# Kernel tuning notes

Measured on AMD Instinct MI355X. Metric: run time of the kernel, lower is better.

## Reference

```python
import jax, jax.numpy as jnp
import numpy as np

B, L, DMQ, DMV = 8, 1024, 512, 512
H, DK, DV, DOUT = 8, 64, 64, 512
EPS = 1e-6


def _layer_norm(x, gamma, beta):
    # LayerNorm over last dim (size H*DK or H*DV), eps=1e-6
    mu = jnp.mean(x, axis=-1, keepdims=True)
    var = jnp.mean(jnp.square(x - mu), axis=-1, keepdims=True)
    return (x - mu) * jax.lax.rsqrt(var + EPS) * gamma + beta


def setup_inputs() -> dict:
    key = jax.random.key(0)
    ks = jax.random.split(key, 20)
    s = 0.02
    return {
        "q": jax.random.normal(ks[0], (B, L, DMQ), jnp.float32),
        "k": jax.random.normal(ks[1], (B, L, DMV), jnp.float32),
        "v": jax.random.normal(ks[2], (B, L, DMV), jnp.float32),
        "Wq": jax.random.normal(ks[3], (DMQ, H * DK), jnp.float32) * s,
        "bq": jnp.zeros((H * DK,), jnp.float32),
        "Wk": jax.random.normal(ks[4], (DMV, H * DK), jnp.float32) * s,
        "bk": jnp.zeros((H * DK,), jnp.float32),
        "Wv": jax.random.normal(ks[5], (DMV, H * DV), jnp.float32) * s,
        "bv": jnp.zeros((H * DV,), jnp.float32),
        "g_q": jnp.ones((H * DK,), jnp.float32),
        "be_q": jnp.zeros((H * DK,), jnp.float32),
        "g_k": jnp.ones((H * DK,), jnp.float32),
        "be_k": jnp.zeros((H * DK,), jnp.float32),
        "g_v": jnp.ones((H * DV,), jnp.float32),
        "be_v": jnp.zeros((H * DV,), jnp.float32),
        "W1": jax.random.normal(ks[6], (H * DV, H * DV), jnp.float32) * s,
        "b1": jnp.zeros((H * DV,), jnp.float32),
        "W2": jax.random.normal(ks[7], (H * DV, DOUT), jnp.float32) * s,
        "b2": jnp.zeros((DOUT,), jnp.float32),
    }


def reference(q, k, v, Wq, bq, Wk, bk, Wv, bv, g_q, be_q, g_k, be_k, g_v, be_v, W1, b1, W2, b2):
    b, lq = q.shape[0], q.shape[1]
    qp = q @ Wq + bq                       # [B, Lq, H*DK]
    kp = k @ Wk + bk                       # [B, Lk, H*DK]
    vp = v @ Wv + bv                       # [B, Lv, H*DV]
    residual = qp.reshape(b, lq, H, DK)
    qn = _layer_norm(qp, g_q, be_q).reshape(b, lq, H, DK)
    kn = _layer_norm(kp, g_k, be_k).reshape(b, -1, H, DK)
    vn = _layer_norm(vp, g_v, be_v).reshape(b, -1, H, DV)
    # scaled dot-product attention (mask=None path)
    scores = jnp.einsum("bqhd,bkhd->bhqk", qn, kn) / jnp.sqrt(jnp.float32(DK))
    attn = jax.nn.softmax(scores, axis=-1)
    out = jnp.einsum("bhqk,bkhd->bqhd", attn, vn).reshape(b, lq, H * DV)
    # 2-layer FFN head: fc1 (ReLU) then fc2
    h = jax.nn.relu(out @ W1 + b1)
    out = h @ W2 + b2                      # [B, Lq, DOUT]
    return (out, residual)
```

## Files before the change

### kernel.cpp

```cpp
#include <hip/hip_runtime.h>
#include <hip/hip_bf16.h>
#include <stdint.h>

typedef unsigned short u16;
typedef __attribute__((ext_vector_type(8))) short bf16x8;
typedef __attribute__((ext_vector_type(4))) float f32x4;
typedef __attribute__((ext_vector_type(16))) float f32x16;

#define NR 8192
#define DM 512
#define NH 8
#define HD 64
#define LQ 1024

#define QSCALE (0.125f * 1.4426950408889634f)
#define SOFF 16.0f

__device__ __forceinline__ u16 f2b(float f) {
    union { float f; uint32_t u; } v; v.f = f;
    uint32_t r = v.u + 0x7fffu + ((v.u >> 16) & 1u);
    return (u16)(r >> 16);
}
__device__ __forceinline__ uint32_t pk2(float lo, float hi) {
    __hip_bfloat162 h = __float22bfloat162_rn(make_float2(lo, hi));
    union { __hip_bfloat162 h; uint32_t u; } c; c.h = h;
    return c.u;
}
__device__ __forceinline__ float b2f(uint32_t lo16) {
    union { uint32_t u; float f; } c; c.u = lo16 << 16; return c.f;
}

__global__ __launch_bounds__(256)
void prep_kernel(const float* __restrict__ q, const float* __restrict__ k,
                 const float* __restrict__ v, u16* __restrict__ qo,
                 u16* __restrict__ ko, u16* __restrict__ vo,
                 const float* __restrict__ W0, const float* __restrict__ W1,
                 const float* __restrict__ W2, const float* __restrict__ W3,
                 const float* __restrict__ W4,
                 u16* __restrict__ T0, u16* __restrict__ T1, u16* __restrict__ T2,
                 u16* __restrict__ T3, u16* __restrict__ T4)
{
    __shared__ float S[64][65];
    const int bid = blockIdx.x;
    if (bid < 6144) {
        const int y = bid >> 11, x = bid & 2047;
        const float* in = y == 0 ? q : y == 1 ? k : v;
        u16* out = y == 0 ? qo : y == 1 ? ko : vo;
        const int i = x * 256 + threadIdx.x;
        const float4* p = (const float4*)in + (size_t)i * 2;
        float4 a = p[0], b = p[1];
        uint4 o;
        o.x = pk2(a.x, a.y);
        o.y = pk2(a.z, a.w);
        o.z = pk2(b.x, b.y);
        o.w = pk2(b.z, b.w);
        ((uint4*)out)[i] = o;
    } else {
        const int id = bid - 6144;
        const int z = id >> 6, idx = id & 63;
        const float* W = z == 0 ? W0 : z == 1 ? W1 : z == 2 ? W2 : z == 3 ? W3 : W4;
        u16* Wt = z == 0 ? T0 : z == 1 ? T1 : z == 2 ? T2 : z == 3 ? T3 : T4;
        const int k0 = (idx >> 3) * 64, n0 = (idx & 7) * 64;
        #pragma unroll
        for (int p = 0; p < 16; ++p) {
            int i = threadIdx.x + p * 256;
            int r = i >> 6, c = i & 63;
            S[r][c] = W[(size_t)(k0 + r) * DM + n0 + c];
        }
        __syncthreads();
        #pragma unroll
        for (int p = 0; p < 16; ++p) {
            int i = threadIdx.x + p * 256;
            int r = i >> 6, c = i & 63;
            Wt[(size_t)(n0 + r) * DM + k0 + c] = f2b(S[c][r]);
        }
    }
}

__global__ __launch_bounds__(256)
void ln_all_kernel(const float* __restrict__ res, const u16* __restrict__ kpb,
                   const u16* __restrict__ vpb,
                   const float* __restrict__ gq, const float* __restrict__ bq,
                   const float* __restrict__ gk, const float* __restrict__ bk,
                   const float* __restrict__ gv, const float* __restrict__ bv,
                   u16* __restrict__ oq, u16* __restrict__ ok,
                   u16* __restrict__ vtb)
{
    __shared__ float ss[4], ss2[4];
    __shared__ u16 S[64][82];
    __shared__ float stats[64][2];
    __shared__ float gb_[512], bb_[512];

    const int bid = blockIdx.x;
    const int t = threadIdx.x;

    if (bid < 16384) {
        const int y = bid >> 13;
        const int row = bid & 8191;
        const float* gm = y == 0 ? gq : gk;
        const float* be = y == 0 ? bq : bk;
        u16* out = y == 0 ? oq : ok;
        const float scale = y == 0 ? QSCALE : 1.f;

        const size_t off = (size_t)row * DM + t * 2;
        float vx, vy;
        if (y == 0) {
            float2 v = *(const float2*)(res + off);
            vx = v.x; vy = v.y;
        } else {
            uint32_t u = *(const uint32_t*)(kpb + off);
            vx = b2f(u & 0xffffu); vy = b2f(u >> 16);
        }
        float s = vx + vy, s2 = vx * vx + vy * vy;
        #pragma unroll
        for (int o = 32; o; o >>= 1) { s += __shfl_down(s, o); s2 += __shfl_down(s2, o); }
        if ((t & 63) == 0) { ss[t >> 6] = s; ss2[t >> 6] = s2; }
        __syncthreads();
        float Sm = ss[0] + ss[1] + ss[2] + ss[3];
        float S2m = ss2[0] + ss2[1] + ss2[2] + ss2[3];
        float mu = Sm * (1.f / DM);
        float var = S2m * (1.f / DM) - mu * mu;
        float rs = rsqrtf(var + 1e-6f);
        float g0 = gm[t * 2] * scale, g1 = gm[t * 2 + 1] * scale;
        float b0 = be[t * 2] * scale, b1 = be[t * 2 + 1] * scale;
        float o0 = (vx - mu) * rs * g0 + b0;
        float o1 = (vy - mu) * rs * g1 + b1;
        *(uint32_t*)(out + off) = pk2(o0, o1);
        return;
    }

    const int id = bid - 16384;
    const int lt = id & 15, b = id >> 4;

    gb_[t]       = gv[t];
    gb_[t + 256] = gv[t + 256];
    bb_[t]       = bv[t];
    bb_[t + 256] = bv[t + 256];

    {
        const int r = t >> 2, qd = t & 3;
        const u16* src = vpb + ((size_t)(b * LQ + lt * 64 + r)) * DM + qd * 8;
        float s = 0.f, s2 = 0.f;
        #pragma unroll
        for (int p = 0; p < 16; ++p) {
            uint4 x = *(const uint4*)(src + p * 32);
            const uint32_t xs[4] = {x.x, x.y, x.z, x.w};
            #pragma unroll
            for (int e = 0; e < 4; ++e) {
                float f0 = b2f(xs[e] & 0xffffu), f1 = b2f(xs[e] >> 16);
                s += f0 + f1; s2 += f0 * f0 + f1 * f1;
            }
        }
        s  += __shfl_xor(s, 1);  s  += __shfl_xor(s, 2);
        s2 += __shfl_xor(s2, 1); s2 += __shfl_xor(s2, 2);
        if (qd == 0) {
            float mu = s * (1.f / DM);
            float var = s2 * (1.f / DM) - mu * mu;
            stats[r][0] = mu;
            stats[r][1] = rsqrtf(var + 1e-6f);
        }
    }
    __syncthreads();

    for (int h = 0; h < NH; ++h) {
        {
            const int rr = t >> 2, dc = (t & 3) * 16;
            const u16* sp = vpb + ((size_t)(b * LQ + lt * 64 + rr)) * DM + h * 64 + dc;
            uint4 a = *(const uint4*)sp;
            uint4 b4 = *(const uint4*)(sp + 8);
            const float mu = stats[rr][0], rs = stats[rr][1];
            const uint32_t xs[8] = {a.x, a.y, a.z, a.w, b4.x, b4.y, b4.z, b4.w};
            #pragma unroll
            for (int e = 0; e < 8; ++e) {
                const int c = h * 64 + dc + e * 2;
                float f0 = (b2f(xs[e] & 0xffffu) - mu) * rs * gb_[c]     + bb_[c];
                float f1 = (b2f(xs[e] >> 16)     - mu) * rs * gb_[c + 1] + bb_[c + 1];
                *(uint32_t*)&S[rr][dc + e * 2] = pk2(f0, f1);
            }
        }
        __syncthreads();
        {
            const int d = t >> 2, lc = (t & 3) * 16;
            u16 tmp[16];
            #pragma unroll
            for (int e = 0; e < 16; ++e) tmp[e] = S[lc + e][d];
            u16* dst = vtb + (((size_t)(b * NH + h) * HD + d) << 10) + lt * 64 + lc;
            *(uint4*)dst       = *(uint4*)&tmp[0];
            *(uint4*)(dst + 8) = *(uint4*)&tmp[8];
        }
        __syncthreads();
    }
}

template<bool RELU, bool OUT_BF16>
__device__ __forceinline__
void gemm_body(const u16* __restrict__ A, const u16* __restrict__ Bt,
               const float* __restrict__ bias, void* __restrict__ Cout)
{
    __shared__ u16 Al[4 * 128 * 8];
    __shared__ u16 Bl[4 * 128 * 8];
    const int t = threadIdx.x;
    const int w = t >> 6, l = t & 63;
    const int m0 = blockIdx.x * 128, n0 = blockIdx.y * 128;
    const int sg = w & 3, sr = (w >> 2) * 64;
    const int wm = w >> 2, wn = w & 3;

    const u16* Ap = A  + (size_t)(m0 + sr + l) * DM + sg * 8;
    const u16* Bp = Bt + (size_t)(n0 + sr + l) * DM + sg * 8;
    const int su = (sg * 128 + sr + l) * 8;

    uint4 ga = *(const uint4*)Ap;
    uint4 gb = *(const uint4*)Bp;

    f32x4 acc[4][2];
    #pragma unroll
    for (int mi = 0; mi < 4; ++mi)
        #pragma unroll
        for (int ni = 0; ni < 2; ++ni)
            acc[mi][ni] = {0.f, 0.f, 0.f, 0.f};

    for (int kb = 0; kb < DM / 32; ++kb) {
        __syncthreads();
        *(uint4*)&Al[su] = ga;
        *(uint4*)&Bl[su] = gb;
        if (kb + 1 < DM / 32) {
            ga = *(const uint4*)(Ap + (kb + 1) * 32);
            gb = *(const uint4*)(Bp + (kb + 1) * 32);
        }
        __syncthreads();
        bf16x8 af[4], bfr[2];
        #pragma unroll
        for (int mi = 0; mi < 4; ++mi)
            af[mi] = *(const bf16x8*)&Al[((l >> 4) * 128 + wm * 64 + mi * 16 + (l & 15)) * 8];
        #pragma unroll
        for (int ni = 0; ni < 2; ++ni)
            bfr[ni] = *(const bf16x8*)&Bl[((l >> 4) * 128 + wn * 32 + ni * 16 + (l & 15)) * 8];
        #pragma unroll
        for (int mi = 0; mi < 4; ++mi)
            #pragma unroll
            for (int ni = 0; ni < 2; ++ni)
                acc[mi][ni] = __builtin_amdgcn_mfma_f32_16x16x32_bf16(af[mi], bfr[ni], acc[mi][ni], 0, 0, 0);
    }

    const int cq = l >> 4, cr = l & 15;
    #pragma unroll
    for (int mi = 0; mi < 4; ++mi) {
        const int row = m0 + wm * 64 + mi * 16 + cq * 4;
        #pragma unroll
        for (int ni = 0; ni < 2; ++ni) {
            const int col = n0 + wn * 32 + ni * 16 + cr;
            const float bb = bias[col];
            #pragma unroll
            for (int j = 0; j < 4; ++j) {
                float vv = acc[mi][ni][j] + bb;
                if (RELU) vv = fmaxf(vv, 0.f);
                if (OUT_BF16) ((u16*)Cout)[(size_t)(row + j) * DM + col] = f2b(vv);
                else          ((float*)Cout)[(size_t)(row + j) * DM + col] = vv;
            }
        }
    }
}

template<bool RELU, bool OUT_BF16>
__global__ __launch_bounds__(512)
void mfma_gemm_kernel(const u16* __restrict__ A, const u16* __restrict__ Bt,
                      const float* __restrict__ bias, void* __restrict__ Cout)
{
    gemm_body<RELU, OUT_BF16>(A, Bt, bias, Cout);
}

__global__ __launch_bounds__(512)
void gemm_qkv_kernel(const u16* __restrict__ qbf, const u16* __restrict__ kbf,
                     const u16* __restrict__ vbf,
                     const u16* __restrict__ WqT, const u16* __restrict__ WkT,
                     const u16* __restrict__ WvT,
                     const float* __restrict__ bq, const float* __restrict__ bk,
                     const float* __restrict__ bv,
                     float* __restrict__ res, u16* __restrict__ kpb,
                     u16* __restrict__ vpb)
{
    __shared__ u16 Al[4 * 128 * 8];
    __shared__ u16 Bl[4 * 128 * 8];
    const int z = blockIdx.z;
    const u16* A    = z == 0 ? qbf : z == 1 ? kbf : vbf;
    const u16* Bt   = z == 0 ? WqT : z == 1 ? WkT : WvT;
    const float* bb = z == 0 ? bq  : z == 1 ? bk  : bv;
    const bool obf  = z != 0;
    u16* ob   = z == 1 ? kpb : vpb;

    const int t = threadIdx.x;
    const int w = t >> 6, l = t & 63;
    const int m0 = blockIdx.x * 128, n0 = blockIdx.y * 128;
    const int sg = w & 3, sr = (w >> 2) * 64;
    const int wm = w >> 2, wn = w & 3;

    const u16* Ap = A  + (size_t)(m0 + sr + l) * DM + sg * 8;
    const u16* Bp = Bt + (size_t)(n0 + sr + l) * DM + sg * 8;
    const int su = (sg * 128 + sr + l) * 8;

    uint4 ga = *(const uint4*)Ap;
    uint4 gb = *(const uint4*)Bp;

    f32x4 acc[4][2];
    #pragma unroll
    for (int mi = 0; mi < 4; ++mi)
        #pragma unroll
        for (int ni = 0; ni < 2; ++ni)
            acc[mi][ni] = {0.f, 0.f, 0.f, 0.f};

    for (int kb = 0; kb < DM / 32; ++kb) {
        __syncthreads();
        *(uint4*)&Al[su] = ga;
        *(uint4*)&Bl[su] = gb;
        if (kb + 1 < DM / 32) {
            ga = *(const uint4*)(Ap + (kb + 1) * 32);
            gb = *(const uint4*)(Bp + (kb + 1) * 32);
        }
        __syncthreads();
        bf16x8 af[4], bfr[2];
        #pragma unroll
        for (int mi = 0; mi < 4; ++mi)
            af[mi] = *(const bf16x8*)&Al[((l >> 4) * 128 + wm * 64 + mi * 16 + (l & 15)) * 8];
        #pragma unroll
        for (int ni = 0; ni < 2; ++ni)
            bfr[ni] = *(const bf16x8*)&Bl[((l >> 4) * 128 + wn * 32 + ni * 16 + (l & 15)) * 8];
        #pragma unroll
        for (int mi = 0; mi < 4; ++mi)
            #pragma unroll
            for (int ni = 0; ni < 2; ++ni)
                acc[mi][ni] = __builtin_amdgcn_mfma_f32_16x16x32_bf16(af[mi], bfr[ni], acc[mi][ni], 0, 0, 0);
    }

    const int cq = l >> 4, cr = l & 15;
    #pragma unroll
    for (int mi = 0; mi < 4; ++mi) {
        const int row = m0 + wm * 64 + mi * 16 + cq * 4;
        #pragma unroll
        for (int ni = 0; ni < 2; ++ni) {
            const int col = n0 + wn * 32 + ni * 16 + cr;
            const float bbv = bb[col];
            #pragma unroll
            for (int j = 0; j < 4; ++j) {
                float vv = acc[mi][ni][j] + bbv;
                if (obf) ob[(size_t)(row + j) * DM + col] = f2b(vv);
                else     res[(size_t)(row + j) * DM + col] = vv;
            }
        }
    }
}

__global__ __launch_bounds__(256, 3)
void attn_mfma_kernel(const u16* __restrict__ qn, const u16* __restrict__ kn,
                      const u16* __restrict__ vt, u16* __restrict__ ab)
{
    __shared__ u16 Kl[2][8 * 64 * 8];
    __shared__ u16 Vl[2][8 * 64 * 8];
    __shared__ u16 Pl[4][8 * 32 * 8];

    const int t = threadIdx.x;
    const int w = t >> 6, l = t & 63;
    const int hi = l >> 5, ln = l & 31;

    const int bid = blockIdx.x;
    const int slot = bid >> 3;
    const int bh = (bid & 7) + 8 * (slot & 7);
    const int qt = slot >> 3;
    const int b = bh >> 3, h = bh & 7;

    const size_t bbase = (size_t)b * LQ * DM + h * HD;
    const int q0 = qt * 128 + w * 32;

    bf16x8 qf[4];
    {
        const u16* qp = qn + bbase + (size_t)(q0 + ln) * DM + hi * 8;
        #pragma unroll
        for (int c = 0; c < 4; ++c)
            qf[c] = *(const bf16x8*)(qp + c * 16);
    }

    const u16* Kg = kn + bbase + (size_t)(t & 63) * DM + (t >> 6) * 8;
    const u16* Vg = vt + (((size_t)bh * HD + (t >> 3)) << 10) + (t & 7) * 8;
    const int svu1 = ((t & 7) * 64 + (t >> 3)) * 8;
    const int svu2 = ((t & 7) * 64 + 32 + (t >> 3)) * 8;
    u16* Pw = &Pl[w][0];

    f32x16 oa0, oa1;
    #pragma unroll
    for (int r = 0; r < 16; ++r) { oa0[r] = 0.f; oa1[r] = 0.f; }
    float lsum = 0.f;

    *(uint4*)&Kl[0][t * 8]         = *(const uint4*)Kg;
    *(uint4*)&Kl[0][(t + 256) * 8] = *(const uint4*)(Kg + 32);
    *(uint4*)&Vl[0][svu1]          = *(const uint4*)Vg;
    *(uint4*)&Vl[0][svu2]          = *(const uint4*)(Vg + (32 << 10));
    uint4 ka1 = *(const uint4*)(Kg + (size_t)64 * DM);
    uint4 ka2 = *(const uint4*)(Kg + (size_t)64 * DM + 32);
    uint4 va1 = *(const uint4*)(Vg + 64);
    uint4 va2 = *(const uint4*)(Vg + (32 << 10) + 64);
    int cur = 0;

    for (int kt = 0; kt < 16; ++kt) {
        __syncthreads();

        f32x16 sa0, sa1;
        #pragma unroll
        for (int r = 0; r < 16; ++r) { sa0[r] = -SOFF; sa1[r] = -SOFF; }
        __builtin_amdgcn_s_setprio(1);
        #pragma unroll
        for (int c = 0; c < 4; ++c) {
            bf16x8 k0 = *(const bf16x8*)&Kl[cur][((c * 2 + hi) * 64 + ln) * 8];
            bf16x8 k1 = *(const bf16x8*)&Kl[cur][((c * 2 + hi) * 64 + 32 + ln) * 8];
            sa0 = __builtin_amdgcn_mfma_f32_32x32x16_bf16(k0, qf[c], sa0, 0, 0, 0);
            sa1 = __builtin_amdgcn_mfma_f32_32x32x16_bf16(k1, qf[c], sa1, 0, 0, 0);
        }
        __builtin_amdgcn_s_setprio(0);

        if (kt < 15) {
            *(uint4*)&Kl[cur ^ 1][t * 8]         = ka1;
            *(uint4*)&Kl[cur ^ 1][(t + 256) * 8] = ka2;
            *(uint4*)&Vl[cur ^ 1][svu1]          = va1;
            *(uint4*)&Vl[cur ^ 1][svu2]          = va2;
            if (kt < 14) {
                ka1 = *(const uint4*)(Kg + (size_t)(kt + 2) * 64 * DM);
                ka2 = *(const uint4*)(Kg + (size_t)(kt + 2) * 64 * DM + 32);
                va1 = *(const uint4*)(Vg + (kt + 2) * 64);
                va2 = *(const uint4*)(Vg + (32 << 10) + (kt + 2) * 64);
            }
        }

        #pragma unroll
        for (int r = 0; r < 16; ++r) {
            sa0[r] = __builtin_amdgcn_exp2f(sa0[r]);
            sa1[r] = __builtin_amdgcn_exp2f(sa1[r]);
            lsum += sa0[r] + sa1[r];
        }

        #pragma unroll
        for (int g0 = 0; g0 < 4; ++g0) {
            uint2 w0, w1;
            w0.x = pk2(sa0[4 * g0],     sa0[4 * g0 + 1]);
            w0.y = pk2(sa0[4 * g0 + 2], sa0[4 * g0 + 3]);
            w1.x = pk2(sa1[4 * g0],     sa1[4 * g0 + 1]);
            w1.y = pk2(sa1[4 * g0 + 2], sa1[4 * g0 + 3]);
            *(uint2*)&Pw[(g0 * 32 + ln) * 8 + 4 * hi]       = w0;
            *(uint2*)&Pw[((g0 + 4) * 32 + ln) * 8 + 4 * hi] = w1;
        }

        __builtin_amdgcn_s_setprio(1);
        #pragma unroll
        for (int ks = 0; ks < 4; ++ks) {
            bf16x8 pa = *(const bf16x8*)&Pw[((ks * 2 + hi) * 32 + ln) * 8];
            bf16x8 v0 = *(const bf16x8*)&Vl[cur][((ks * 2 + hi) * 64 + ln) * 8];
            bf16x8 v1 = *(const bf16x8*)&Vl[cur][((ks * 2 + hi) * 64 + 32 + ln) * 8];
            oa0 = __builtin_amdgcn_mfma_f32_32x32x16_bf16(v0, pa, oa0, 0, 0, 0);
            oa1 = __builtin_amdgcn_mfma_f32_32x32x16_bf16(v1, pa, oa1, 0, 0, 0);
        }
        __builtin_amdgcn_s_setprio(0);
        cur ^= 1;
    }

    lsum += __shfl_xor(lsum, 32, 64);
    const float rinv = 1.f / lsum;
    u16* op = ab + (size_t)(b * LQ + q0 + ln) * DM + h * HD;
    #pragma unroll
    for (int g = 0; g < 4; ++g) {
        uint2 s0, s1;
        s0.x = pk2(oa0[4 * g] * rinv, oa0[4 * g + 1] * rinv);
        s0.y = pk2(oa0[4 * g + 2] * rinv, oa0[4 * g + 3] * rinv);
        s1.x = pk2(oa1[4 * g] * rinv, oa1[4 * g + 1] * rinv);
        s1.y = pk2(oa1[4 * g + 2] * rinv, oa1[4 * g + 3] * rinv);
        *(uint2*)(op + 8 * g + 4 * hi)      = s0;
        *(uint2*)(op + 32 + 8 * g + 4 * hi) = s1;
    }
}

extern "C" void kernel_launch(void* const* d_in, const int* in_sizes, int n_in,
                              void* d_out, int out_size, void* d_ws, size_t ws_size,
                              hipStream_t stream)
{
    const float* q    = (const float*)d_in[0];
    const float* k    = (const float*)d_in[1];
    const float* v    = (const float*)d_in[2];
    const float* Wq   = (const float*)d_in[3];
    const float* bq   = (const float*)d_in[4];
    const float* Wk   = (const float*)d_in[5];
    const float* bk   = (const float*)d_in[6];
    const float* Wv   = (const float*)d_in[7];
    const float* bv   = (const float*)d_in[8];
    const float* g_q  = (const float*)d_in[9];
    const float* be_q = (const float*)d_in[10];
    const float* g_k  = (const float*)d_in[11];
    const float* be_k = (const float*)d_in[12];
    const float* g_v  = (const float*)d_in[13];
    const float* be_v = (const float*)d_in[14];
    const float* W1   = (const float*)d_in[15];
    const float* b1   = (const float*)d_in[16];
    const float* W2   = (const float*)d_in[17];
    const float* b2   = (const float*)d_in[18];

    float* outp = (float*)d_out;
    float* res  = outp + (size_t)NR * DM;

    char* wsb = (char*)d_ws;
    const size_t MB = 1024 * 1024;
    u16* kpb = (u16*)(wsb);
    u16* vpb = (u16*)(wsb + 8 * MB);
    u16* hbb = (u16*)(wsb + 16 * MB);
    u16* vtb = (u16*)(wsb + 24 * MB);
    u16* qbf = (u16*)(wsb + 32 * MB);
    u16* kbf = (u16*)(wsb + 40 * MB);
    u16* vbf = (u16*)(wsb + 48 * MB);
    u16* WqT = (u16*)(wsb + 56 * MB);
    u16* WkT = WqT + 512 * 512;
    u16* WvT = WkT + 512 * 512;
    u16* W1T = WvT + 512 * 512;
    u16* W2T = W1T + 512 * 512;
    u16* abb = (u16*)wsb;

    prep_kernel<<<6464, 256, 0, stream>>>(q, k, v, qbf, kbf, vbf,
                                          Wq, Wk, Wv, W1, W2,
                                          WqT, WkT, WvT, W1T, W2T);

    gemm_qkv_kernel<<<dim3(NR / 128, DM / 128, 3), 512, 0, stream>>>(
        qbf, kbf, vbf, WqT, WkT, WvT, bq, bk, bv, res, kpb, vpb);

    ln_all_kernel<<<16384 + 128, 256, 0, stream>>>(res, kpb, vpb,
                                                   g_q, be_q, g_k, be_k, g_v, be_v,
                                                   qbf, kbf, vtb);

    attn_mfma_kernel<<<512, 256, 0, stream>>>(qbf, kbf, vtb, abb);

    dim3 gg(NR / 128, DM / 128);
    mfma_gemm_kernel<true,  true ><<<gg, 512, 0, stream>>>(abb, W1T, b1, (void*)hbb);
    mfma_gemm_kernel<false, false><<<gg, 512, 0, stream>>>(hbb, W2T, b2, (void*)outp);
}
```

Before: 122.7 us.

## Fuse fp32-to-bf16 input conversion into QKV GEMM and use direct global-to-LDS loads

Drops the separate pass that converts q/k/v to bf16. The QKV GEMM now reads fp32 activations and converts them in registers before staging them in LDS, which removes a full write and re-read of three bf16 activation tensors. B-operand and the FFN GEMM tiles are loaded with global_load_lds directly into shared memory instead of through registers, giving up the register-level prefetch of the next k-block. Each fp32 A tile is now re-read by every N-block, so A read traffic doubles in bytes.

Measured after the change: 134.9 us. 1.1x slower.

```diff
diff --git a/kernel.cpp b/kernel.cpp
--- a/kernel.cpp
+++ b/kernel.cpp
@@ -16,6 +16,10 @@
 #define QSCALE (0.125f * 1.4426950408889634f)
 #define SOFF 16.0f
 
+#define GLOAD16(g, l) __builtin_amdgcn_global_load_lds(                     \
+    (const __attribute__((address_space(1))) void*)(g),                     \
+    (__attribute__((address_space(3))) void*)(l), 16, 0, 0)
+
 __device__ __forceinline__ u16 f2b(float f) {
     union { float f; uint32_t u; } v; v.f = f;
     uint32_t r = v.u + 0x7fffu + ((v.u >> 16) & 1u);
@@ -31,49 +35,30 @@
 }
 
 __global__ __launch_bounds__(256)
-void prep_kernel(const float* __restrict__ q, const float* __restrict__ k,
-                 const float* __restrict__ v, u16* __restrict__ qo,
-                 u16* __restrict__ ko, u16* __restrict__ vo,
-                 const float* __restrict__ W0, const float* __restrict__ W1,
+void prep_kernel(const float* __restrict__ W0, const float* __restrict__ W1,
                  const float* __restrict__ W2, const float* __restrict__ W3,
                  const float* __restrict__ W4,
                  u16* __restrict__ T0, u16* __restrict__ T1, u16* __restrict__ T2,
                  u16* __restrict__ T3, u16* __restrict__ T4)
 {
     __shared__ float S[64][65];
-    const int bid = blockIdx.x;
-    if (bid < 6144) {
-        const int y = bid >> 11, x = bid & 2047;
-        const float* in = y == 0 ? q : y == 1 ? k : v;
-        u16* out = y == 0 ? qo : y == 1 ? ko : vo;
-        const int i = x * 256 + threadIdx.x;
-        const float4* p = (const float4*)in + (size_t)i * 2;
-        float4 a = p[0], b = p[1];
-        uint4 o;
-        o.x = pk2(a.x, a.y);
-        o.y = pk2(a.z, a.w);
-        o.z = pk2(b.x, b.y);
-        o.w = pk2(b.z, b.w);
-        ((uint4*)out)[i] = o;
-    } else {
-        const int id = bid - 6144;
-        const int z = id >> 6, idx = id & 63;
-        const float* W = z == 0 ? W0 : z == 1 ? W1 : z == 2 ? W2 : z == 3 ? W3 : W4;
-        u16* Wt = z == 0 ? T0 : z == 1 ? T1 : z == 2 ? T2 : z == 3 ? T3 : T4;
-        const int k0 = (idx >> 3) * 64, n0 = (idx & 7) * 64;
-        #pragma unroll
-        for (int p = 0; p < 16; ++p) {
-            int i = threadIdx.x + p * 256;
-            int r = i >> 6, c = i & 63;
-            S[r][c] = W[(size_t)(k0 + r) * DM + n0 + c];
-        }
-        __syncthreads();
-        #pragma unroll
-        for (int p = 0; p < 16; ++p) {
-            int i = threadIdx.x + p * 256;
-            int r = i >> 6, c = i & 63;
-            Wt[(size_t)(n0 + r) * DM + k0 + c] = f2b(S[c][r]);
-        }
+    const int id = blockIdx.x;
+    const int z = id >> 6, idx = id & 63;
+    const float* W = z == 0 ? W0 : z == 1 ? W1 : z == 2 ? W2 : z == 3 ? W3 : W4;
+    u16* Wt = z == 0 ? T0 : z == 1 ? T1 : z == 2 ? T2 : z == 3 ? T3 : T4;
+    const int k0 = (idx >> 3) * 64, n0 = (idx & 7) * 64;
+    #pragma unroll
+    for (int p = 0; p < 16; ++p) {
+        int i = threadIdx.x + p * 256;
+        int r = i >> 6, c = i & 63;
+        S[r][c] = W[(size_t)(k0 + r) * DM + n0 + c];
+    }
+    __syncthreads();
+    #pragma unroll
+    for (int p = 0; p < 16; ++p) {
+        int i = threadIdx.x + p * 256;
+        int r = i >> 6, c = i & 63;
+        Wt[(size_t)(n0 + r) * DM + k0 + c] = f2b(S[c][r]);
     }
 }
 
@@ -193,9 +178,9 @@
 }
 
 template<bool RELU, bool OUT_BF16>
-__device__ __forceinline__
-void gemm_body(const u16* __restrict__ A, const u16* __restrict__ Bt,
-               const float* __restrict__ bias, void* __restrict__ Cout)
+__global__ __launch_bounds__(512)
+void mfma_gemm_kernel(const u16* __restrict__ A, const u16* __restrict__ Bt,
+                      const float* __restrict__ bias, void* __restrict__ Cout)
 {
     __shared__ u16 Al[4 * 128 * 8];
     __shared__ u16 Bl[4 * 128 * 8];
@@ -207,10 +192,8 @@
 
     const u16* Ap = A  + (size_t)(m0 + sr + l) * DM + sg * 8;
     const u16* Bp = Bt + (size_t)(n0 + sr + l) * DM + sg * 8;
-    const int su = (sg * 128 + sr + l) * 8;
-
-    uint4 ga = *(const uint4*)Ap;
-    uint4 gb = *(const uint4*)Bp;
+    u16* Alp = &Al[(sg * 128 + sr + l) * 8];
+    u16* Blp = &Bl[(sg * 128 + sr + l) * 8];
 
     f32x4 acc[4][2];
     #pragma unroll
@@ -221,12 +204,8 @@
 
     for (int kb = 0; kb < DM / 32; ++kb) {
         __syncthreads();
-        *(uint4*)&Al[su] = ga;
-        *(uint4*)&Bl[su] = gb;
-        if (kb + 1 < DM / 32) {
-            ga = *(const uint4*)(Ap + (kb + 1) * 32);
-            gb = *(const uint4*)(Bp + (kb + 1) * 32);
-        }
+        GLOAD16(Ap + kb * 32, Alp);
+        GLOAD16(Bp + kb * 32, Blp);
         __syncthreads();
         bf16x8 af[4], bfr[2];
         #pragma unroll
@@ -261,17 +240,9 @@
     }
 }
 
-template<bool RELU, bool OUT_BF16>
 __global__ __launch_bounds__(512)
-void mfma_gemm_kernel(const u16* __restrict__ A, const u16* __restrict__ Bt,
-                      const float* __restrict__ bias, void* __restrict__ Cout)
-{
-    gemm_body<RELU, OUT_BF16>(A, Bt, bias, Cout);
-}
-
-__global__ __launch_bounds__(512)
-void gemm_qkv_kernel(const u16* __restrict__ qbf, const u16* __restrict__ kbf,
-                     const u16* __restrict__ vbf,
+void gemm_qkv_kernel(const float* __restrict__ qf32, const float* __restrict__ kf32,
+                     const float* __restrict__ vf32,
                      const u16* __restrict__ WqT, const u16* __restrict__ WkT,
                      const u16* __restrict__ WvT,
                      const float* __restrict__ bq, const float* __restrict__ bk,
@@ -282,7 +253,7 @@
     __shared__ u16 Al[4 * 128 * 8];
     __shared__ u16 Bl[4 * 128 * 8];
     const int z = blockIdx.z;
-    const u16* A    = z == 0 ? qbf : z == 1 ? kbf : vbf;
+    const float* A  = z == 0 ? qf32 : z == 1 ? kf32 : vf32;
     const u16* Bt   = z == 0 ? WqT : z == 1 ? WkT : WvT;
     const float* bb = z == 0 ? bq  : z == 1 ? bk  : bv;
     const bool obf  = z != 0;
@@ -294,12 +265,13 @@
     const int sg = w & 3, sr = (w >> 2) * 64;
     const int wm = w >> 2, wn = w & 3;
 
-    const u16* Ap = A  + (size_t)(m0 + sr + l) * DM + sg * 8;
+    const float* Ap = A + (size_t)(m0 + sr + l) * DM + sg * 8;
     const u16* Bp = Bt + (size_t)(n0 + sr + l) * DM + sg * 8;
-    const int su = (sg * 128 + sr + l) * 8;
-
-    uint4 ga = *(const uint4*)Ap;
-    uint4 gb = *(const uint4*)Bp;
+    u16* Alp = &Al[(sg * 128 + sr + l) * 8];
+    u16* Blp = &Bl[(sg * 128 + sr + l) * 8];
+
+    float4 fa = *(const float4*)Ap;
+    float4 fb = *(const float4*)(Ap + 4);
 
     f32x4 acc[4][2];
     #pragma unroll
@@ -310,11 +282,14 @@
 
     for (int kb = 0; kb < DM / 32; ++kb) {
         __syncthreads();
-        *(uint4*)&Al[su] = ga;
-        *(uint4*)&Bl[su] = gb;
+        uint4 aw;
+        aw.x = pk2(fa.x, fa.y); aw.y = pk2(fa.z, fa.w);
+        aw.z = pk2(fb.x, fb.y); aw.w = pk2(fb.z, fb.w);
+        *(uint4*)Alp = aw;
+        GLOAD16(Bp + kb * 32, Blp);
         if (kb + 1 < DM / 32) {
-            ga = *(const uint4*)(Ap + (kb + 1) * 32);
-            gb = *(const uint4*)(Bp + (kb + 1) * 32);
+            fa = *(const float4*)(Ap + (kb + 1) * 32);
+            fb = *(const float4*)(Ap + (kb + 1) * 32 + 4);
         }
         __syncthreads();
         bf16x8 af[4], bfr[2];
@@ -509,7 +484,6 @@
     u16* vtb = (u16*)(wsb + 24 * MB);
     u16* qbf = (u16*)(wsb + 32 * MB);
     u16* kbf = (u16*)(wsb + 40 * MB);
-    u16* vbf = (u16*)(wsb + 48 * MB);
     u16* WqT = (u16*)(wsb + 56 * MB);
     u16* WkT = WqT + 512 * 512;
     u16* WvT = WkT + 512 * 512;
@@ -517,12 +491,11 @@
     u16* W2T = W1T + 512 * 512;
     u16* abb = (u16*)wsb;
 
-    prep_kernel<<<6464, 256, 0, stream>>>(q, k, v, qbf, kbf, vbf,
-                                          Wq, Wk, Wv, W1, W2,
-                                          WqT, WkT, WvT, W1T, W2T);
+    prep_kernel<<<320, 256, 0, stream>>>(Wq, Wk, Wv, W1, W2,
+                                         WqT, WkT, WvT, W1T, W2T);
 
     gemm_qkv_kernel<<<dim3(NR / 128, DM / 128, 3), 512, 0, stream>>>(
-        qbf, kbf, vbf, WqT, WkT, WvT, bq, bk, bv, res, kpb, vpb);
+        q, k, v, WqT, WkT, WvT, bq, bk, bv, res, kpb, vpb);
 
     ln_all_kernel<<<16384 + 128, 256, 0, stream>>>(res, kpb, vpb,
                                                    g_q, be_q, g_k, be_k, g_v, be_v,
```
